# Kernel optimization log

Measured on AMD Instinct MI355X. Metric: run time of the kernel, lower is better.

The kernel has to match this reference:

```python
import jax, jax.numpy as jnp
import numpy as np

E = 8          # num_experts
K = 2          # top_k
R = 16         # lora_r
SCALING = 32.0 / 16.0  # lora_alpha / lora_r

B, S, H, I = 2, 2048, 2048, 8192


def setup_inputs() -> dict:
    key = jax.random.key(0)
    ks = jax.random.split(key, 11)
    inv_h = 1.0 / np.sqrt(H)
    inv_i = 1.0 / np.sqrt(I)
    return {
        "x": jax.random.normal(ks[0], (B, S, H), jnp.float32),
        "gate_W": jax.random.normal(ks[1], (I, H), jnp.float32) * inv_h,
        "up_W": jax.random.normal(ks[2], (I, H), jnp.float32) * inv_h,
        "down_W": jax.random.normal(ks[3], (H, I), jnp.float32) * inv_i,
        "router_W": jax.random.normal(ks[4], (E, H), jnp.float32) * 0.02,
        "gate_A": jax.random.normal(ks[5], (E, R, H), jnp.float32) * inv_h,
        "gate_B": jax.random.normal(ks[6], (E, I, R), jnp.float32) * 0.01,
        "up_A": jax.random.normal(ks[7], (E, R, H), jnp.float32) * inv_h,
        "up_B": jax.random.normal(ks[8], (E, I, R), jnp.float32) * 0.01,
        "down_A": jax.random.normal(ks[9], (E, R, I), jnp.float32) * inv_i,
        "down_B": jax.random.normal(ks[10], (E, H, R), jnp.float32) * 0.01,
    }


def _mixlora_forward(x, gate_W, up_W, down_W, router_W,
                     gate_A, gate_B, up_A, up_B, down_A, down_B):
    b, s, h = x.shape
    T = b * s
    xf = x.reshape(T, h)                                  # [T, H]

    # Shared base FFN projections (computed once for all experts)
    gate_out = xf @ gate_W.T                              # [T, I]
    up_out = xf @ up_W.T                                  # [T, I]

    # Router: softmax in fp32, top-k, renormalize selected weights
    logits = xf @ router_W.T                              # [T, E]
    probs = jax.nn.softmax(logits.astype(jnp.float32), axis=-1)
    w, idx = jax.lax.top_k(probs, K)                      # [T, K]
    w = w / jnp.sum(w, axis=-1, keepdims=True)

    # Dense per-(token, expert) combine weights; 0 for unselected experts
    onehot = jax.nn.one_hot(idx, E, dtype=probs.dtype)    # [T, K, E]
    w_dense = jnp.einsum('tke,tk->te', onehot, w)         # [T, E]

    # Load-balance aux loss: N * sum_i f_i * P_i
    f_i = jnp.sum(onehot, axis=(0, 1)) / T
    p_i = jnp.mean(probs, axis=0)
    aux_loss = E * jnp.dot(f_i, p_i)

    # Scan over experts, accumulating weighted intermediate and down-delta.
    # Since down_proj is linear, sum_k w_k * down(inter_k) = down(sum_k w_k * inter_k).
    def step(carry, p):
        acc_int, acc_dd = carry
        gA, gB, uA, uB, dA, dB, we = p                    # we: [T]
        gd = ((xf @ gA.T) @ gB.T) * SCALING               # [T, I]
        ud = ((xf @ uA.T) @ uB.T) * SCALING               # [T, I]
        inter = jax.nn.silu(gate_out + gd) * (up_out + ud)  # SwiGLU intermediate
        dd = ((inter @ dA.T) @ dB.T) * SCALING            # [T, H]
        we = we.astype(xf.dtype)[:, None]
        return (acc_int + we * inter, acc_dd + we * dd), None

    init = (jnp.zeros((T, gate_W.shape[0]), xf.dtype),
            jnp.zeros((T, h), xf.dtype))
    (acc_int, acc_dd), _ = jax.lax.scan(
        step, init, (gate_A, gate_B, up_A, up_B, down_A, down_B, w_dense.T))

    out = acc_int @ down_W.T + acc_dd                     # [T, H]
    return out.reshape(b, s, h), aux_loss


def reference(x, gate_W, up_W, down_W, router_W,
              gate_A, gate_B, up_A, up_B, down_A, down_B):
    return _mixlora_forward(x, gate_W, up_W, down_W, router_W,
                            gate_A, gate_B, up_A, up_B, down_A, down_B)
```

## Files before the change

### kernel.cpp

```cpp
#include <hip/hip_runtime.h>
#include <stdint.h>
#include <stddef.h>

#define DEVINL __device__ __forceinline__

typedef short sv8 __attribute__((ext_vector_type(8)));
typedef unsigned short usv8 __attribute__((ext_vector_type(8)));
typedef unsigned short usv4 __attribute__((ext_vector_type(4)));
typedef float f32x4 __attribute__((ext_vector_type(4)));

constexpr int T_TOK = 4096;
constexpr int H_DIM = 2048;
constexpr int I_DIM = 8192;
constexpr int E_NUM = 8;
constexpr int R_LORA = 16;
constexpr float SCALING = 2.0f;
constexpr int NQ = 4;
constexpr int TQ = T_TOK / NQ;
constexpr int PQ = TQ * 2;
constexpr int P_TOT = T_TOK * 2;

DEVINL float bf2f(unsigned short u) {
  union { uint32_t i; float f; } v; v.i = ((uint32_t)u) << 16; return v.f;
}
DEVINL unsigned short f2bf(float x) {
  union { float f; uint32_t i; } v; v.f = x;
  uint32_t r = v.i + 0x7FFFu + ((v.i >> 16) & 1u);
  return (unsigned short)(r >> 16);
}
DEVINL float bflo(uint32_t w) {
  union { uint32_t i; float f; } v; v.i = w << 16; return v.f;
}
DEVINL float bfhi(uint32_t w) {
  union { uint32_t i; float f; } v; v.i = w & 0xFFFF0000u; return v.f;
}

DEVINL f32x4 MFMA_BF16(sv8 a, sv8 b, f32x4 c) {
  return __builtin_amdgcn_mfma_f32_16x16x32_bf16(a, b, c, 0, 0, 0);
}

DEVINL void load16_to_lds(const void* g, void* l) {
  __builtin_amdgcn_global_load_lds(
      (const __attribute__((address_space(1))) uint32_t*)g,
      (__attribute__((address_space(3))) uint32_t*)l, 16, 0, 0);
}

#define BARRIER() __builtin_amdgcn_s_barrier()

__global__ void cast_f32_to_bf16(const float4* __restrict__ src, usv4* __restrict__ dst) {
  long i = (long)blockIdx.x * blockDim.x + threadIdx.x;
  float4 v = src[i];
  usv4 o;
  o[0] = f2bf(v.x); o[1] = f2bf(v.y); o[2] = f2bf(v.z); o[3] = f2bf(v.w);
  dst[i] = o;
}

__global__ void zero_lcnt(int* lcnt) {
  if (threadIdx.x < E_NUM * NQ) lcnt[threadIdx.x] = 0;
}

__global__ void router_kernel(const float* __restrict__ x, const float* __restrict__ rW,
                              float* __restrict__ wbuf, int* __restrict__ idxb,
                              float* __restrict__ probs, int* __restrict__ lcnt,
                              int* __restrict__ lists, unsigned short* __restrict__ xf_bf) {
  const int wave = threadIdx.x >> 6, lane = threadIdx.x & 63;
  const int t = blockIdx.x * 4 + wave;
  const float* xr = x + (long)t * H_DIM;
  unsigned short* xbr = xf_bf + (long)t * H_DIM;
  float acc[E_NUM];
#pragma unroll
  for (int e = 0; e < E_NUM; ++e) acc[e] = 0.f;
  for (int h = lane; h < H_DIM; h += 64) {
    float xv = xr[h];
    xbr[h] = f2bf(xv);
#pragma unroll
    for (int e = 0; e < E_NUM; ++e) acc[e] += xv * rW[e * H_DIM + h];
  }
#pragma unroll
  for (int e = 0; e < E_NUM; ++e) {
#pragma unroll
    for (int off = 32; off; off >>= 1) acc[e] += __shfl_xor(acc[e], off);
  }
  if (lane == 0) {
    float mx = acc[0];
#pragma unroll
    for (int e = 1; e < E_NUM; ++e) mx = fmaxf(mx, acc[e]);
    float p[E_NUM];
    float s = 0.f;
#pragma unroll
    for (int e = 0; e < E_NUM; ++e) { p[e] = expf(acc[e] - mx); s += p[e]; }
    float inv = 1.f / s;
#pragma unroll
    for (int e = 0; e < E_NUM; ++e) p[e] *= inv;
    int e1 = 0;
    for (int e = 1; e < E_NUM; ++e) if (p[e] > p[e1]) e1 = e;
    int e2 = (e1 == 0) ? 1 : 0;
    for (int e = 0; e < E_NUM; ++e) if (e != e1 && p[e] > p[e2]) e2 = e;
    float w1 = p[e1], w2 = p[e2], wsum = w1 + w2;
    wbuf[t * 2 + 0] = w1 / wsum;
    wbuf[t * 2 + 1] = w2 / wsum;
    idxb[t * 2 + 0] = e1;
    idxb[t * 2 + 1] = e2;
#pragma unroll
    for (int e = 0; e < E_NUM; ++e) probs[(long)t * E_NUM + e] = p[e];
    const int q = t / TQ;
    int p1 = atomicAdd(&lcnt[e1 * NQ + q], 1); lists[(e1 * NQ + q) * TQ + p1] = t * 2 + 0;
    int p2 = atomicAdd(&lcnt[e2 * NQ + q], 1); lists[(e2 * NQ + q) * TQ + p2] = t * 2 + 1;
  }
}

__global__ void aux_kernel(const float* __restrict__ probs, const int* __restrict__ lcnt,
                           float* __restrict__ aux_out) {
  const int lane = threadIdx.x;
  float s[E_NUM];
#pragma unroll
  for (int e = 0; e < E_NUM; ++e) s[e] = 0.f;
  for (int t = lane; t < T_TOK; t += 64) {
#pragma unroll
    for (int e = 0; e < E_NUM; ++e) s[e] += probs[(long)t * E_NUM + e];
  }
#pragma unroll
  for (int e = 0; e < E_NUM; ++e) {
#pragma unroll
    for (int off = 32; off; off >>= 1) s[e] += __shfl_xor(s[e], off);
  }
  if (lane == 0) {
    float a = 0.f;
#pragma unroll
    for (int e = 0; e < E_NUM; ++e) {
      int cnt = 0;
#pragma unroll
      for (int q = 0; q < NQ; ++q) cnt += lcnt[e * NQ + q];
      a += ((float)cnt / (float)T_TOK) * (s[e] / (float)T_TOK);
    }
    *aux_out = (float)E_NUM * a;
  }
}

__global__ __launch_bounds__(256)
void lora_a_mfma_kernel(const unsigned short* __restrict__ xf_bf,
                        const unsigned short* __restrict__ gA_bf,
                        const unsigned short* __restrict__ uA_bf,
                        const int* __restrict__ lists, const int* __restrict__ lcnt,
                        float* __restrict__ vg, float* __restrict__ vu) {
  const int q = blockIdx.x / (E_NUM * 16);
  const int rem = blockIdx.x % (E_NUM * 16);
  const int e = rem >> 4;
  const int wave = threadIdx.x >> 6, lane = threadIdx.x & 63;
  const int grp = (rem & 15) * 4 + wave;
  const int npairs = lcnt[e * NQ + q];
  if (grp * 16 >= npairs) return;
  const int* lst = lists + (e * NQ + q) * TQ;
  const int slot = lane & 15;
  int pidx = grp * 16 + slot;
  int pair = lst[(pidx < npairs) ? pidx : grp * 16];
  int t = pair >> 1;
  const long kb = (long)blockIdx.y * 1024 + (lane >> 4) * 8;
  const unsigned short* arow = xf_bf + (long)t * H_DIM + kb;
  const unsigned short* bg = gA_bf + ((long)e * R_LORA + slot) * H_DIM + kb;
  const unsigned short* bu = uA_bf + ((long)e * R_LORA + slot) * H_DIM + kb;
  f32x4 ag = {}, au = {};
#pragma unroll 4
  for (int k = 0; k < 1024; k += 32) {
    sv8 a = *(const sv8*)(arow + k);
    ag = MFMA_BF16(a, *(const sv8*)(bg + k), ag);
    au = MFMA_BF16(a, *(const sv8*)(bu + k), au);
  }
  const int orow = (lane >> 4) * 4;
  const long base = (long)blockIdx.y * P_TOT;
#pragma unroll
  for (int rg = 0; rg < 4; ++rg) {
    int pidx2 = grp * 16 + orow + rg;
    if (pidx2 < npairs) {
      int pr = lst[pidx2];
      vg[(base + pr) * R_LORA + slot] = ag[rg];
      vu[(base + pr) * R_LORA + slot] = au[rg];
    }
  }
}

__global__ void reduce_uguu_kernel(const float* __restrict__ vg, const float* __restrict__ vu,
                                   float* __restrict__ ug, float* __restrict__ uu) {
  long i = (long)blockIdx.x * 256 + threadIdx.x;
  ug[i] = vg[i] + vg[(long)P_TOT * R_LORA + i];
  uu[i] = vu[i] + vu[(long)P_TOT * R_LORA + i];
}

template <bool F32OUT>
__global__ __launch_bounds__(512, 2)
void gemm8p_t(const unsigned short* __restrict__ A,
              const unsigned short* __restrict__ B0,
              const unsigned short* __restrict__ B1,
              unsigned short* __restrict__ Cb0,
              unsigned short* __restrict__ Cb1,
              float* __restrict__ Cf,
              int K, int lda, int ldb, int ldc,
              int az_off, int bz_off, long cz_off) {
  extern __shared__ unsigned short lds[];
  const int z = blockIdx.z;
  const unsigned short* __restrict__ Ap = A + (long)z * az_off;
  const unsigned short* __restrict__ Bp = (z ? B1 : B0) + (long)z * bz_off;
  const int tid = threadIdx.x;
  const int wave = tid >> 6, lane = tid & 63;
  const int wm = wave >> 2, wn = wave & 3;
  const long m0 = (long)blockIdx.y * 256;
  const long n0 = (long)blockIdx.x * 256;
  const int NT = K >> 6;

  const int lr = lane & 15;
  const int lc = (lane >> 4) * 8;
  const int xm = ((lane & 4) << 3) | ((lane & 2) << 3) | ((lane & 1) << 6);
  const int srow = tid >> 3;
  const int scol = (tid & 7) * 8;
  const int gcol = scol ^ (((tid >> 5) & 1) << 4) ^ (((tid >> 4) & 1) << 3)
                        ^ (((tid >> 3) & 1) << 5);

  f32x4 acc[8][4] = {};
  sv8 aF[4][2], bF[4][2];

  auto ldsAt = [&](int buf, int mat) -> unsigned short* {
    return lds + (((buf << 1) + mat) << 14);
  };
  auto stageA = [&](int buf, int R, long k0) {
    load16_to_lds(Ap + (m0 + R + srow) * (long)lda + k0 + gcol,
                  ldsAt(buf, 0) + ((R + srow) << 6) + scol);
  };
  auto stageB = [&](int buf, int R, long k0) {
    load16_to_lds(Bp + (n0 + R + srow) * (long)ldb + k0 + gcol,
                  ldsAt(buf, 1) + ((R + srow) << 6) + scol);
  };
  auto rdA = [&](int buf, int row16, int ks) -> sv8 {
    int bo = ((((row16 + lr) << 7) + ((ks * 32 + lc) << 1))) ^ xm;
    return *(const sv8*)((const char*)ldsAt(buf, 0) + bo);
  };
  auto rdB = [&](int buf, int row16, int ks) -> sv8 {
    int bo = ((((row16 + lr) << 7) + ((ks * 32 + lc) << 1))) ^ xm;
    return *(const sv8*)((const char*)ldsAt(buf, 1) + bo);
  };

  stageA(0, 0, 0); stageA(0, 64, 0); stageA(0, 128, 0); stageA(0, 192, 0);
  stageB(0, 0, 0); stageB(0, 64, 0); stageB(0, 128, 0); stageB(0, 192, 0);
  if (NT > 1) {
    stageA(1, 0, 64); stageA(1, 128, 64);
    stageB(1, 0, 64); stageB(1, 64, 64);
    stageA(1, 64, 64); stageA(1, 192, 64);
    asm volatile("s_waitcnt vmcnt(6)" ::: "memory");
  } else {
    asm volatile("s_waitcnt vmcnt(0)" ::: "memory");
  }
  BARRIER();

  for (int t = 0; t < NT; ++t) {
    const int P = t & 1, Q = P ^ 1;
    const long kN1 = ((long)t + 1) << 6;
    const long kN2 = ((long)t + 2) << 6;
    const bool s1 = (t + 1) < NT;
    const bool s2 = (t + 2) < NT;

#pragma unroll
    for (int mf = 0; mf < 4; ++mf)
#pragma unroll
      for (int ks = 0; ks < 2; ++ks)
        aF[mf][ks] = rdA(P, wm * 128 + mf * 16, ks);
#pragma unroll
    for (int nf = 0; nf < 2; ++nf)
#pragma unroll
      for (int ks = 0; ks < 2; ++ks)
        bF[nf][ks] = rdB(P, wn * 64 + nf * 16, ks);
    if (s1) { stageB(Q, 128, kN1); stageB(Q, 192, kN1); }
    BARRIER();
    __builtin_amdgcn_s_setprio(1);
#pragma unroll
    for (int mf = 0; mf < 4; ++mf)
#pragma unroll
      for (int nf = 0; nf < 2; ++nf)
#pragma unroll
        for (int ks = 0; ks < 2; ++ks)
          acc[mf][nf] = MFMA_BF16(aF[mf][ks], bF[nf][ks], acc[mf][nf]);
    __builtin_amdgcn_s_setprio(0);
    BARRIER();

#pragma unroll
    for (int nf = 0; nf < 2; ++nf)
#pragma unroll
      for (int ks = 0; ks < 2; ++ks)
        bF[2 + nf][ks] = rdB(P, wn * 64 + (2 + nf) * 16, ks);
    if (s2) { stageA(P, 0, kN2); stageA(P, 128, kN2); }
    BARRIER();
    __builtin_amdgcn_s_setprio(1);
#pragma unroll
    for (int mf = 0; mf < 4; ++mf)
#pragma unroll
      for (int nf = 0; nf < 2; ++nf)
#pragma unroll
        for (int ks = 0; ks < 2; ++ks)
          acc[mf][2 + nf] = MFMA_BF16(aF[mf][ks], bF[2 + nf][ks], acc[mf][2 + nf]);
    __builtin_amdgcn_s_setprio(0);
    BARRIER();

#pragma unroll
    for (int mf = 0; mf < 4; ++mf)
#pragma unroll
      for (int ks = 0; ks < 2; ++ks)
        aF[mf][ks] = rdA(P, wm * 128 + 64 + mf * 16, ks);
    if (s2) { stageB(P, 0, kN2); stageB(P, 64, kN2); }
    BARRIER();
    __builtin_amdgcn_s_setprio(1);
#pragma unroll
    for (int mf = 0; mf < 4; ++mf)
#pragma unroll
      for (int nf = 0; nf < 2; ++nf)
#pragma unroll
        for (int ks = 0; ks < 2; ++ks)
          acc[4 + mf][nf] = MFMA_BF16(aF[mf][ks], bF[nf][ks], acc[4 + mf][nf]);
    __builtin_amdgcn_s_setprio(0);
    BARRIER();

    if (s2) {
      stageA(P, 64, kN2); stageA(P, 192, kN2);
      asm volatile("s_waitcnt vmcnt(6)" ::: "memory");
    } else {
      asm volatile("s_waitcnt vmcnt(0)" ::: "memory");
    }
    BARRIER();
    __builtin_amdgcn_s_setprio(1);
#pragma unroll
    for (int mf = 0; mf < 4; ++mf)
#pragma unroll
      for (int nf = 0; nf < 2; ++nf)
#pragma unroll
        for (int ks = 0; ks < 2; ++ks)
          acc[4 + mf][2 + nf] = MFMA_BF16(aF[mf][ks], bF[2 + nf][ks], acc[4 + mf][2 + nf]);
    __builtin_amdgcn_s_setprio(0);
    BARRIER();
  }

  const int rb = (lane >> 4) * 4, cb = lane & 15;
  if constexpr (F32OUT) {
    float* __restrict__ Cp = Cf + (long)z * cz_off;
#pragma unroll
    for (int mf = 0; mf < 8; ++mf)
#pragma unroll
      for (int nf = 0; nf < 4; ++nf) {
        long col = n0 + wn * 64 + nf * 16 + cb;
#pragma unroll
        for (int r = 0; r < 4; ++r) {
          long row = m0 + wm * 128 + mf * 16 + rb + r;
          Cp[row * ldc + col] = acc[mf][nf][r];
        }
      }
  } else {
    unsigned short* __restrict__ Cp = z ? Cb1 : Cb0;
#pragma unroll
    for (int mf = 0; mf < 8; ++mf)
#pragma unroll
      for (int nf = 0; nf < 4; ++nf) {
        long col = n0 + wn * 64 + nf * 16 + cb;
#pragma unroll
        for (int r = 0; r < 4; ++r) {
          long row = m0 + wm * 128 + mf * 16 + rb + r;
          Cp[row * ldc + col] = f2bf(acc[mf][nf][r]);
        }
      }
  }
}

__global__ __launch_bounds__(256)
void combine2_kernel(const unsigned short* __restrict__ g_bf,
                     const unsigned short* __restrict__ u_bf,
                     const float* __restrict__ gB, const float* __restrict__ uB,
                     const float* __restrict__ ug, const float* __restrict__ uu,
                     const float* __restrict__ wbuf,
                     const int* __restrict__ lists, const int* __restrict__ lcnt,
                     unsigned short* __restrict__ winter, int q) {
  const int e = blockIdx.y >> 4, chunk = blockIdx.y & 15;
  const int npairs = lcnt[e * NQ + q];
  const int pbase = chunk * 64;
  if (pbase >= npairs) return;
  const int wave = threadIdx.x >> 6, lane = threadIdx.x & 63;
  const long i0 = (long)blockIdx.x * 256 + lane * 4;
  uint32_t gbp[32], ubp[32];
#pragma unroll
  for (int j = 0; j < 4; ++j) {
    const float4* gp = (const float4*)(gB + ((long)e * I_DIM + i0 + j) * R_LORA);
    const float4* up = (const float4*)(uB + ((long)e * I_DIM + i0 + j) * R_LORA);
#pragma unroll
    for (int c = 0; c < 4; ++c) {
      float4 gv = gp[c], uv = up[c];
      gbp[j * 8 + c * 2 + 0] = (uint32_t)f2bf(gv.x) | ((uint32_t)f2bf(gv.y) << 16);
      gbp[j * 8 + c * 2 + 1] = (uint32_t)f2bf(gv.z) | ((uint32_t)f2bf(gv.w) << 16);
      ubp[j * 8 + c * 2 + 0] = (uint32_t)f2bf(uv.x) | ((uint32_t)f2bf(uv.y) << 16);
      ubp[j * 8 + c * 2 + 1] = (uint32_t)f2bf(uv.z) | ((uint32_t)f2bf(uv.w) << 16);
    }
  }
  for (int pl = 0; pl < 16; ++pl) {
    int pi = pbase + wave + pl * 4;
    if (pi >= npairs) break;
    int pair = lists[(e * NQ + q) * TQ + pi];
    int t = pair >> 1, plocal = pair - q * PQ;
    float w = wbuf[pair];
    const float2* ug2 = (const float2*)(ug + (long)pair * R_LORA);
    const float2* uu2 = (const float2*)(uu + (long)pair * R_LORA);
    usv4 gv = *(const usv4*)(g_bf + (long)t * I_DIM + i0);
    usv4 uv = *(const usv4*)(u_bf + (long)t * I_DIM + i0);
    float gd[4] = {0.f, 0.f, 0.f, 0.f}, ud[4] = {0.f, 0.f, 0.f, 0.f};
#pragma unroll
    for (int c = 0; c < 8; ++c) {
      float2 a = ug2[c], b = uu2[c];
#pragma unroll
      for (int j = 0; j < 4; ++j) {
        uint32_t gw = gbp[j * 8 + c], uw = ubp[j * 8 + c];
        gd[j] += a.x * bflo(gw) + a.y * bfhi(gw);
        ud[j] += b.x * bflo(uw) + b.y * bfhi(uw);
      }
    }
    usv4 o;
#pragma unroll
    for (int j = 0; j < 4; ++j) {
      float zg = bf2f(gv[j]) + SCALING * gd[j];
      float zu = bf2f(uv[j]) + SCALING * ud[j];
      float sil = zg / (1.f + __expf(-zg));
      o[j] = f2bf(w * sil * zu);
    }
    *(usv4*)(winter + (long)plocal * I_DIM + i0) = o;
  }
}

__global__ void acc_kernel(const unsigned short* __restrict__ winter,
                           unsigned short* __restrict__ acc_bf, int q) {
  long gid = (long)blockIdx.x * 256 + threadIdx.x;
  int tl = (int)(gid >> 10);
  int ig = (int)(gid & 1023);
  int t = q * TQ + tl;
  usv8 a = *(const usv8*)(winter + ((long)(tl * 2 + 0)) * I_DIM + ig * 8);
  usv8 b = *(const usv8*)(winter + ((long)(tl * 2 + 1)) * I_DIM + ig * 8);
  usv8 o;
#pragma unroll
  for (int j = 0; j < 8; ++j) o[j] = f2bf(bf2f(a[j]) + bf2f(b[j]));
  *(usv8*)(acc_bf + (long)t * I_DIM + ig * 8) = o;
}

__global__ __launch_bounds__(256)
void lorav_mfma_kernel(const unsigned short* __restrict__ winter,
                       const unsigned short* __restrict__ dA_bf,
                       const int* __restrict__ lists, const int* __restrict__ lcnt,
                       float* __restrict__ vv, int q) {
  const int e = blockIdx.x >> 4;
  const int wave = threadIdx.x >> 6, lane = threadIdx.x & 63;
  const int grp = (blockIdx.x & 15) * 4 + wave;
  const int npairs = lcnt[e * NQ + q];
  if (grp * 16 >= npairs) return;
  const int* lst = lists + (e * NQ + q) * TQ;
  const int slot = lane & 15;
  int pidx = grp * 16 + slot;
  int pair = lst[(pidx < npairs) ? pidx : grp * 16];
  int plocal = pair - q * PQ;
  const long kb = (long)blockIdx.y * 1024 + (lane >> 4) * 8;
  const unsigned short* arow = winter + (long)plocal * I_DIM + kb;
  const unsigned short* brow = dA_bf + ((long)e * R_LORA + slot) * I_DIM + kb;
  f32x4 acc = {};
#pragma unroll 4
  for (int k = 0; k < 1024; k += 32)
    acc = MFMA_BF16(*(const sv8*)(arow + k), *(const sv8*)(brow + k), acc);
  const int orow = (lane >> 4) * 4;
  const long base = (long)blockIdx.y * P_TOT;
#pragma unroll
  for (int rg = 0; rg < 4; ++rg) {
    int pidx2 = grp * 16 + orow + rg;
    if (pidx2 < npairs) {
      int pr = lst[pidx2];
      vv[(base + pr) * R_LORA + slot] = acc[rg];
    }
  }
}

__global__ void reduce_v_kernel(const float* __restrict__ vv, float* __restrict__ vbuf) {
  long i = (long)blockIdx.x * 256 + threadIdx.x;
  float s = 0.f;
#pragma unroll
  for (int kc = 0; kc < 8; ++kc) s += vv[(long)kc * P_TOT * R_LORA + i];
  vbuf[i] = s;
}

__global__ void dd_kernel(const float* __restrict__ vbuf, const int* __restrict__ idxb,
                          const float* __restrict__ dB,
                          float* __restrict__ out) {
  const int t = blockIdx.y;
  const int h = blockIdx.x * 256 + threadIdx.x;
  const int e0 = idxb[t * 2 + 0], e1 = idxb[t * 2 + 1];
  const float4* v0p = (const float4*)(vbuf + (long)(t * 2 + 0) * R_LORA);
  const float4* v1p = (const float4*)(vbuf + (long)(t * 2 + 1) * R_LORA);
  const float4* b0 = (const float4*)(dB + ((long)e0 * H_DIM + h) * R_LORA);
  const float4* b1 = (const float4*)(dB + ((long)e1 * H_DIM + h) * R_LORA);
  float dd = 0.f;
#pragma unroll
  for (int qq = 0; qq < 4; ++qq) {
    float4 v0 = v0p[qq], x0 = b0[qq];
    float4 v1 = v1p[qq], x1 = b1[qq];
    dd += v0.x * x0.x + v0.y * x0.y + v0.z * x0.z + v0.w * x0.w;
    dd += v1.x * x1.x + v1.y * x1.y + v1.z * x1.z + v1.w * x1.w;
  }
  out[(long)t * H_DIM + h] = SCALING * dd;
}

__global__ void merge_out_kernel(const float4* __restrict__ p0, const float4* __restrict__ p1,
                                 float4* __restrict__ out) {
  long i = (long)blockIdx.x * 256 + threadIdx.x;
  float4 a = p0[i], b = p1[i], o = out[i];
  o.x += a.x + b.x; o.y += a.y + b.y; o.z += a.z + b.z; o.w += a.w + b.w;
  out[i] = o;
}

extern "C" void kernel_launch(void* const* d_in, const int* in_sizes, int n_in,
                              void* d_out, int out_size, void* d_ws, size_t ws_size,
                              hipStream_t stream) {
  (void)in_sizes; (void)n_in; (void)out_size;
  const float* x        = (const float*)d_in[0];
  const float* gate_W   = (const float*)d_in[1];
  const float* up_W     = (const float*)d_in[2];
  const float* down_W   = (const float*)d_in[3];
  const float* router_W = (const float*)d_in[4];
  const float* gate_A   = (const float*)d_in[5];
  const float* gate_B   = (const float*)d_in[6];
  const float* up_A     = (const float*)d_in[7];
  const float* up_B     = (const float*)d_in[8];
  const float* down_A   = (const float*)d_in[9];
  const float* down_B   = (const float*)d_in[10];
  float* out = (float*)d_out;

  char* ws = (char*)d_ws;
  size_t off = 0;
  auto take = [&](size_t bytes) -> char* {
    char* p = ws + off;
    off += (bytes + 255) & ~(size_t)255;
    return p;
  };
  unsigned short* xf_bf  = (unsigned short*)take((size_t)T_TOK * H_DIM * 2);
  unsigned short* gW_bf  = (unsigned short*)take((size_t)I_DIM * H_DIM * 2);
  unsigned short* uW_bf  = (unsigned short*)take((size_t)I_DIM * H_DIM * 2);
  unsigned short* dA_bf  = (unsigned short*)take((size_t)E_NUM * R_LORA * I_DIM * 2);
  unsigned short* g_bf   = (unsigned short*)take((size_t)T_TOK * I_DIM * 2);
  unsigned short* u_bf   = (unsigned short*)take((size_t)T_TOK * I_DIM * 2);
  unsigned short* winterQ= (unsigned short*)take((size_t)PQ * I_DIM * 2);
  float* wbuf  = (float*)take((size_t)P_TOT * 4);
  int*   idxb  = (int*)take((size_t)P_TOT * 4);
  float* ug    = (float*)take((size_t)P_TOT * R_LORA * 4);
  float* uu    = (float*)take((size_t)P_TOT * R_LORA * 4);
  float* vbuf  = (float*)take((size_t)P_TOT * R_LORA * 4);
  float* probs = (float*)take((size_t)T_TOK * E_NUM * 4);
  int*   lcnt  = (int*)take((size_t)E_NUM * NQ * 4);
  int*   lists = (int*)take((size_t)E_NUM * NQ * TQ * 4);

  unsigned short* dW_bf  = gW_bf;
  unsigned short* acc_bf = g_bf;
  float* vg = (float*)winterQ;
  float* vu = (float*)(winterQ + (size_t)1 * 1024 * 1024 / 2);
  unsigned short* gA_bf = winterQ + (size_t)2 * 1024 * 1024 / 2;
  unsigned short* uA_bf = winterQ + (size_t)5 * 512 * 1024 / 2;
  float* vv = (float*)xf_bf;
  float* pbuf = (float*)u_bf;

  if (ws_size < off) return;

  zero_lcnt<<<1, 64, 0, stream>>>(lcnt);
  router_kernel<<<T_TOK / 4, 256, 0, stream>>>(x, router_W, wbuf, idxb, probs, lcnt, lists, xf_bf);
  aux_kernel<<<1, 64, 0, stream>>>(probs, lcnt, out + (size_t)T_TOK * H_DIM);

  cast_f32_to_bf16<<<(E_NUM * R_LORA * H_DIM / 4) / 256, 256, 0, stream>>>((const float4*)gate_A, (usv4*)gA_bf);
  cast_f32_to_bf16<<<(E_NUM * R_LORA * H_DIM / 4) / 256, 256, 0, stream>>>((const float4*)up_A, (usv4*)uA_bf);
  lora_a_mfma_kernel<<<dim3(NQ * E_NUM * 16, 2), 256, 0, stream>>>(xf_bf, gA_bf, uA_bf, lists, lcnt, vg, vu);
  reduce_uguu_kernel<<<(P_TOT * R_LORA) / 256, 256, 0, stream>>>(vg, vu, ug, uu);

  cast_f32_to_bf16<<<(I_DIM * H_DIM / 4) / 256, 256, 0, stream>>>((const float4*)gate_W, (usv4*)gW_bf);
  cast_f32_to_bf16<<<(I_DIM * H_DIM / 4) / 256, 256, 0, stream>>>((const float4*)up_W, (usv4*)uW_bf);
  cast_f32_to_bf16<<<(E_NUM * R_LORA * I_DIM / 4) / 256, 256, 0, stream>>>((const float4*)down_A, (usv4*)dA_bf);

  hipFuncSetAttribute(reinterpret_cast<const void*>(&gemm8p_t<false>),
                      hipFuncAttributeMaxDynamicSharedMemorySize, 131072);
  hipFuncSetAttribute(reinterpret_cast<const void*>(&gemm8p_t<true>),
                      hipFuncAttributeMaxDynamicSharedMemorySize, 131072);
  gemm8p_t<false><<<dim3(I_DIM / 256, T_TOK / 256, 2), 512, 131072, stream>>>(
      xf_bf, gW_bf, uW_bf, g_bf, u_bf, nullptr,
      H_DIM, H_DIM, H_DIM, I_DIM, 0, 0, 0);

  cast_f32_to_bf16<<<(H_DIM * I_DIM / 4) / 256, 256, 0, stream>>>((const float4*)down_W, (usv4*)dW_bf);

  for (int q = 0; q < NQ; ++q) {
    combine2_kernel<<<dim3(I_DIM / 256, E_NUM * 16), 256, 0, stream>>>(
        g_bf, u_bf, gate_B, up_B, ug, uu, wbuf, lists, lcnt, winterQ, q);
    acc_kernel<<<(TQ * (I_DIM / 8)) / 256, 256, 0, stream>>>(winterQ, acc_bf, q);
    lorav_mfma_kernel<<<dim3(E_NUM * 16, 8), 256, 0, stream>>>(winterQ, dA_bf, lists, lcnt, vv, q);
  }
  reduce_v_kernel<<<(P_TOT * R_LORA) / 256, 256, 0, stream>>>(vv, vbuf);

  dd_kernel<<<dim3(H_DIM / 256, T_TOK), 256, 0, stream>>>(vbuf, idxb, down_B, out);

  gemm8p_t<true><<<dim3(H_DIM / 256, T_TOK / 256, 2), 512, 131072, stream>>>(
      acc_bf, dW_bf, dW_bf, nullptr, nullptr, pbuf,
      I_DIM / 2, I_DIM, I_DIM, H_DIM, I_DIM / 2, I_DIM / 2, (long)T_TOK * H_DIM);
  merge_out_kernel<<<(T_TOK * H_DIM / 4) / 256, 256, 0, stream>>>(
      (const float4*)pbuf, (const float4*)(pbuf + (size_t)T_TOK * H_DIM), (float4*)out);
}
```

Measured before the change: 1.139 ms.

## Prefetch GEMM LDS fragments across iterations, pre-cast LoRA B, fuse dd with merge

The main GEMM loop is restructured with separate A-fragment and B-fragment register sets. The next iteration's first A/B fragments are read from LDS during the last MFMA phase of the current iteration, so LDS read latency can overlap with compute. Separately, gate_B and up_B are cast to bf16 once up front, so combine2 no longer converts them from fp32 on every one of its four launches. The dd kernel is also merged with the final output merge kernel, which removes a full read-modify-write pass over the output. The cost is more register pressure in the GEMM and extra workspace aliasing inside xf_bf.

```diff
diff --git a/kernel.cpp b/kernel.cpp
--- a/kernel.cpp
+++ b/kernel.cpp
@@ -46,6 +46,7 @@
 }
 
 #define BARRIER() __builtin_amdgcn_s_barrier()
+#define SB0() __builtin_amdgcn_sched_barrier(0)
 
 __global__ void cast_f32_to_bf16(const float4* __restrict__ src, usv4* __restrict__ dst) {
   long i = (long)blockIdx.x * blockDim.x + threadIdx.x;
@@ -216,7 +217,7 @@
                         ^ (((tid >> 3) & 1) << 5);
 
   f32x4 acc[8][4] = {};
-  sv8 aF[4][2], bF[4][2];
+  sv8 A1[4][2], A2[4][2], bLo[2][2], bHi[2][2];
 
   auto ldsAt = [&](int buf, int mat) -> unsigned short* {
     return lds + (((buf << 1) + mat) << 14);
@@ -249,25 +250,47 @@
     asm volatile("s_waitcnt vmcnt(0)" ::: "memory");
   }
   BARRIER();
+#pragma unroll
+  for (int mf = 0; mf < 4; ++mf)
+#pragma unroll
+    for (int ks = 0; ks < 2; ++ks)
+      A2[mf][ks] = rdA(0, wm * 128 + mf * 16, ks);
+#pragma unroll
+  for (int nf = 0; nf < 2; ++nf)
+#pragma unroll
+    for (int ks = 0; ks < 2; ++ks)
+      bLo[nf][ks] = rdB(0, wn * 64 + nf * 16, ks);
 
   for (int t = 0; t < NT; ++t) {
     const int P = t & 1, Q = P ^ 1;
     const long kN1 = ((long)t + 1) << 6;
     const long kN2 = ((long)t + 2) << 6;
-    const bool s1 = (t + 1) < NT;
-    const bool s2 = (t + 2) < NT;
-
+    const bool s1 = (t + 1) < NT, s2 = (t + 2) < NT;
+
+#pragma unroll
+    for (int nf = 0; nf < 2; ++nf)
+#pragma unroll
+      for (int ks = 0; ks < 2; ++ks)
+        bHi[nf][ks] = rdB(P, wn * 64 + (2 + nf) * 16, ks);
+    if (s1) { stageB(Q, 128, kN1); stageB(Q, 192, kN1); }
+    BARRIER();
+    __builtin_amdgcn_s_setprio(1);
 #pragma unroll
     for (int mf = 0; mf < 4; ++mf)
 #pragma unroll
+      for (int nf = 0; nf < 2; ++nf)
+#pragma unroll
+        for (int ks = 0; ks < 2; ++ks)
+          acc[mf][nf] = MFMA_BF16(A2[mf][ks], bLo[nf][ks], acc[mf][nf]);
+    __builtin_amdgcn_s_setprio(0);
+    BARRIER();
+
+#pragma unroll
+    for (int mf = 0; mf < 4; ++mf)
+#pragma unroll
       for (int ks = 0; ks < 2; ++ks)
-        aF[mf][ks] = rdA(P, wm * 128 + mf * 16, ks);
-#pragma unroll
-    for (int nf = 0; nf < 2; ++nf)
-#pragma unroll
-      for (int ks = 0; ks < 2; ++ks)
-        bF[nf][ks] = rdB(P, wn * 64 + nf * 16, ks);
-    if (s1) { stageB(Q, 128, kN1); stageB(Q, 192, kN1); }
+        A1[mf][ks] = rdA(P, wm * 128 + 64 + mf * 16, ks);
+    if (s2) { stageA(P, 0, kN2); stageA(P, 128, kN2); }
     BARRIER();
     __builtin_amdgcn_s_setprio(1);
 #pragma unroll
@@ -276,16 +299,11 @@
       for (int nf = 0; nf < 2; ++nf)
 #pragma unroll
         for (int ks = 0; ks < 2; ++ks)
-          acc[mf][nf] = MFMA_BF16(aF[mf][ks], bF[nf][ks], acc[mf][nf]);
+          acc[mf][2 + nf] = MFMA_BF16(A2[mf][ks], bHi[nf][ks], acc[mf][2 + nf]);
     __builtin_amdgcn_s_setprio(0);
     BARRIER();
 
-#pragma unroll
-    for (int nf = 0; nf < 2; ++nf)
-#pragma unroll
-      for (int ks = 0; ks < 2; ++ks)
-        bF[2 + nf][ks] = rdB(P, wn * 64 + (2 + nf) * 16, ks);
-    if (s2) { stageA(P, 0, kN2); stageA(P, 128, kN2); }
+    if (s2) { stageB(P, 0, kN2); stageB(P, 64, kN2); }
     BARRIER();
     __builtin_amdgcn_s_setprio(1);
 #pragma unroll
@@ -294,25 +312,7 @@
       for (int nf = 0; nf < 2; ++nf)
 #pragma unroll
         for (int ks = 0; ks < 2; ++ks)
-          acc[mf][2 + nf] = MFMA_BF16(aF[mf][ks], bF[2 + nf][ks], acc[mf][2 + nf]);
-    __builtin_amdgcn_s_setprio(0);
-    BARRIER();
-
-#pragma unroll
-    for (int mf = 0; mf < 4; ++mf)
-#pragma unroll
-      for (int ks = 0; ks < 2; ++ks)
-        aF[mf][ks] = rdA(P, wm * 128 + 64 + mf * 16, ks);
-    if (s2) { stageB(P, 0, kN2); stageB(P, 64, kN2); }
-    BARRIER();
-    __builtin_amdgcn_s_setprio(1);
-#pragma unroll
-    for (int mf = 0; mf < 4; ++mf)
-#pragma unroll
-      for (int nf = 0; nf < 2; ++nf)
-#pragma unroll
-        for (int ks = 0; ks < 2; ++ks)
-          acc[4 + mf][nf] = MFMA_BF16(aF[mf][ks], bF[nf][ks], acc[4 + mf][nf]);
+          acc[4 + mf][nf] = MFMA_BF16(A1[mf][ks], bLo[nf][ks], acc[4 + mf][nf]);
     __builtin_amdgcn_s_setprio(0);
     BARRIER();
 
@@ -323,6 +323,19 @@
       asm volatile("s_waitcnt vmcnt(0)" ::: "memory");
     }
     BARRIER();
+    SB0();
+    if (s1) {
+#pragma unroll
+      for (int mf = 0; mf < 4; ++mf)
+#pragma unroll
+        for (int ks = 0; ks < 2; ++ks)
+          A2[mf][ks] = rdA(Q, wm * 128 + mf * 16, ks);
+#pragma unroll
+      for (int nf = 0; nf < 2; ++nf)
+#pragma unroll
+        for (int ks = 0; ks < 2; ++ks)
+          bLo[nf][ks] = rdB(Q, wn * 64 + nf * 16, ks);
+    }
     __builtin_amdgcn_s_setprio(1);
 #pragma unroll
     for (int mf = 0; mf < 4; ++mf)
@@ -330,7 +343,7 @@
       for (int nf = 0; nf < 2; ++nf)
 #pragma unroll
         for (int ks = 0; ks < 2; ++ks)
-          acc[4 + mf][2 + nf] = MFMA_BF16(aF[mf][ks], bF[2 + nf][ks], acc[4 + mf][2 + nf]);
+          acc[4 + mf][2 + nf] = MFMA_BF16(A1[mf][ks], bHi[nf][ks], acc[4 + mf][2 + nf]);
     __builtin_amdgcn_s_setprio(0);
     BARRIER();
   }
@@ -368,7 +381,7 @@
 __global__ __launch_bounds__(256)
 void combine2_kernel(const unsigned short* __restrict__ g_bf,
                      const unsigned short* __restrict__ u_bf,
-                     const float* __restrict__ gB, const float* __restrict__ uB,
+                     const unsigned short* __restrict__ gBp, const unsigned short* __restrict__ uBp,
                      const float* __restrict__ ug, const float* __restrict__ uu,
                      const float* __restrict__ wbuf,
                      const int* __restrict__ lists, const int* __restrict__ lcnt,
@@ -382,16 +395,13 @@
   uint32_t gbp[32], ubp[32];
 #pragma unroll
   for (int j = 0; j < 4; ++j) {
-    const float4* gp = (const float4*)(gB + ((long)e * I_DIM + i0 + j) * R_LORA);
-    const float4* up = (const float4*)(uB + ((long)e * I_DIM + i0 + j) * R_LORA);
-#pragma unroll
-    for (int c = 0; c < 4; ++c) {
-      float4 gv = gp[c], uv = up[c];
-      gbp[j * 8 + c * 2 + 0] = (uint32_t)f2bf(gv.x) | ((uint32_t)f2bf(gv.y) << 16);
-      gbp[j * 8 + c * 2 + 1] = (uint32_t)f2bf(gv.z) | ((uint32_t)f2bf(gv.w) << 16);
-      ubp[j * 8 + c * 2 + 0] = (uint32_t)f2bf(uv.x) | ((uint32_t)f2bf(uv.y) << 16);
-      ubp[j * 8 + c * 2 + 1] = (uint32_t)f2bf(uv.z) | ((uint32_t)f2bf(uv.w) << 16);
-    }
+    const uint4* gp = (const uint4*)(gBp + ((long)e * I_DIM + i0 + j) * R_LORA);
+    const uint4* up = (const uint4*)(uBp + ((long)e * I_DIM + i0 + j) * R_LORA);
+    uint4 g0 = gp[0], g1 = gp[1], u0 = up[0], u1 = up[1];
+    gbp[j * 8 + 0] = g0.x; gbp[j * 8 + 1] = g0.y; gbp[j * 8 + 2] = g0.z; gbp[j * 8 + 3] = g0.w;
+    gbp[j * 8 + 4] = g1.x; gbp[j * 8 + 5] = g1.y; gbp[j * 8 + 6] = g1.z; gbp[j * 8 + 7] = g1.w;
+    ubp[j * 8 + 0] = u0.x; ubp[j * 8 + 1] = u0.y; ubp[j * 8 + 2] = u0.z; ubp[j * 8 + 3] = u0.w;
+    ubp[j * 8 + 4] = u1.x; ubp[j * 8 + 5] = u1.y; ubp[j * 8 + 6] = u1.z; ubp[j * 8 + 7] = u1.w;
   }
   for (int pl = 0; pl < 16; ++pl) {
     int pi = pbase + wave + pl * 4;
@@ -482,9 +492,10 @@
   vbuf[i] = s;
 }
 
-__global__ void dd_kernel(const float* __restrict__ vbuf, const int* __restrict__ idxb,
-                          const float* __restrict__ dB,
-                          float* __restrict__ out) {
+__global__ void ddmerge_kernel(const float* __restrict__ vbuf, const int* __restrict__ idxb,
+                               const float* __restrict__ dB,
+                               const float* __restrict__ p0, const float* __restrict__ p1,
+                               float* __restrict__ out) {
   const int t = blockIdx.y;
   const int h = blockIdx.x * 256 + threadIdx.x;
   const int e0 = idxb[t * 2 + 0], e1 = idxb[t * 2 + 1];
@@ -500,15 +511,8 @@
     dd += v0.x * x0.x + v0.y * x0.y + v0.z * x0.z + v0.w * x0.w;
     dd += v1.x * x1.x + v1.y * x1.y + v1.z * x1.z + v1.w * x1.w;
   }
-  out[(long)t * H_DIM + h] = SCALING * dd;
-}
-
-__global__ void merge_out_kernel(const float4* __restrict__ p0, const float4* __restrict__ p1,
-                                 float4* __restrict__ out) {
-  long i = (long)blockIdx.x * 256 + threadIdx.x;
-  float4 a = p0[i], b = p1[i], o = out[i];
-  o.x += a.x + b.x; o.y += a.y + b.y; o.z += a.z + b.z; o.w += a.w + b.w;
-  out[i] = o;
+  long i = (long)t * H_DIM + h;
+  out[i] = SCALING * dd + p0[i] + p1[i];
 }
 
 extern "C" void kernel_launch(void* const* d_in, const int* in_sizes, int n_in,
@@ -558,6 +562,8 @@
   unsigned short* gA_bf = winterQ + (size_t)2 * 1024 * 1024 / 2;
   unsigned short* uA_bf = winterQ + (size_t)5 * 512 * 1024 / 2;
   float* vv = (float*)xf_bf;
+  unsigned short* gB_bf = (unsigned short*)((char*)xf_bf + ((size_t)4 << 20));
+  unsigned short* uB_bf = (unsigned short*)((char*)xf_bf + ((size_t)8 << 20));
   float* pbuf = (float*)u_bf;
 
   if (ws_size < off) return;
@@ -584,20 +590,22 @@
       H_DIM, H_DIM, H_DIM, I_DIM, 0, 0, 0);
 
   cast_f32_to_bf16<<<(H_DIM * I_DIM / 4) / 256, 256, 0, stream>>>((const float4*)down_W, (usv4*)dW_bf);
+  cast_f32_to_bf16<<<(E_NUM * I_DIM * R_LORA / 4) / 256, 256, 0, stream>>>((const float4*)gate_B, (usv4*)gB_bf);
+  cast_f32_to_bf16<<<(E_NUM * I_DIM * R_LORA / 4) / 256, 256, 0, stream>>>((const float4*)up_B, (usv4*)uB_bf);
 
   for (int q = 0; q < NQ; ++q) {
     combine2_kernel<<<dim3(I_DIM / 256, E_NUM * 16), 256, 0, stream>>>(
-        g_bf, u_bf, gate_B, up_B, ug, uu, wbuf, lists, lcnt, winterQ, q);
+        g_bf, u_bf, gB_bf, uB_bf, ug, uu, wbuf, lists, lcnt, winterQ, q);
     acc_kernel<<<(TQ * (I_DIM / 8)) / 256, 256, 0, stream>>>(winterQ, acc_bf, q);
     lorav_mfma_kernel<<<dim3(E_NUM * 16, 8), 256, 0, stream>>>(winterQ, dA_bf, lists, lcnt, vv, q);
   }
   reduce_v_kernel<<<(P_TOT * R_LORA) / 256, 256, 0, stream>>>(vv, vbuf);
-
-  dd_kernel<<<dim3(H_DIM / 256, T_TOK), 256, 0, stream>>>(vbuf, idxb, down_B, out);
 
   gemm8p_t<true><<<dim3(H_DIM / 256, T_TOK / 256, 2), 512, 131072, stream>>>(
       acc_bf, dW_bf, dW_bf, nullptr, nullptr, pbuf,
       I_DIM / 2, I_DIM, I_DIM, H_DIM, I_DIM / 2, I_DIM / 2, (long)T_TOK * H_DIM);
-  merge_out_kernel<<<(T_TOK * H_DIM / 4) / 256, 256, 0, stream>>>(
-      (const float4*)pbuf, (const float4*)(pbuf + (size_t)T_TOK * H_DIM), (float4*)out);
-}
+
+  ddmerge_kernel<<<dim3(H_DIM / 256, T_TOK), 256, 0, stream>>>(
+      vbuf, idxb, down_B, (const float*)pbuf,
+      (const float*)(pbuf + (size_t)T_TOK * H_DIM), out);
+}
```

Result: slower. 1.298 ms (+14.0%).
